# Kernel tuning notes

Measured on AMD Instinct MI355X. Metric: run time of the kernel, lower is better.

Reference implementation:

```python
import jax, jax.numpy as jnp
import numpy as np

VOCAB = 50000
WORD_DIM = 300
ENT_DIM = 128
ATT_DIM = 256
B, QLEN, DLEN = 64, 32, 2048
MUS = np.array([-0.9, -0.7, -0.5, -0.3, -0.1, 0.1, 0.3, 0.5, 0.7, 0.9, 1.0], dtype=np.float32)
SIGMAS = np.array([0.1] * 10 + [0.001], dtype=np.float32)


def setup_inputs() -> dict:
    key = jax.random.key(0)
    ks = jax.random.split(key, 12)
    # tokens in [-1, VOCAB-2]; -1 is padding (embed uses tok+1)
    query_tok = jax.random.randint(ks[0], (B, QLEN), -1, VOCAB - 1)
    doc_tok = jax.random.randint(ks[1], (B, DLEN), -1, VOCAB - 1)
    query_entity = jax.random.normal(ks[2], (B, QLEN, ENT_DIM), dtype=jnp.float32)
    doc_entity = jax.random.normal(ks[3], (B, DLEN, ENT_DIM), dtype=jnp.float32)
    embed_table = jax.random.normal(ks[4], (VOCAB, WORD_DIM), dtype=jnp.float32) * 0.1
    W_t = jax.random.normal(ks[5], (WORD_DIM, ATT_DIM), dtype=jnp.float32) * (1.0 / np.sqrt(WORD_DIM))
    b_t = jax.random.normal(ks[6], (ATT_DIM,), dtype=jnp.float32) * 0.01
    W_e = jax.random.normal(ks[7], (ENT_DIM, ATT_DIM), dtype=jnp.float32) * (1.0 / np.sqrt(ENT_DIM))
    b_e = jax.random.normal(ks[8], (ATT_DIM,), dtype=jnp.float32) * 0.01
    W_c = jax.random.normal(ks[9], (len(MUS), 1), dtype=jnp.float32) * 0.3
    b_c = jax.random.normal(ks[10], (1,), dtype=jnp.float32) * 0.01
    return {
        "query_tok": query_tok, "doc_tok": doc_tok,
        "query_entity": query_entity, "doc_entity": doc_entity,
        "embed_table": embed_table,
        "W_t": W_t, "b_t": b_t, "W_e": W_e, "b_e": b_e,
        "W_c": W_c, "b_c": b_c,
    }


def reference(query_tok, doc_tok, query_entity, doc_entity,
              embed_table, W_t, b_t, W_e, b_e, W_c, b_c):
    mus = jnp.asarray(MUS)
    sigmas = jnp.asarray(SIGMAS)
    # encode: embed(tok + 1)
    q_reps = embed_table[query_tok + 1]            # [B,Q,WORD]
    d_reps = embed_table[doc_tok + 1]              # [B,D,WORD]
    # transform_embed: relu(Linear(word) + Linear(entity))
    q = jax.nn.relu(q_reps @ W_t + b_t + query_entity @ W_e + b_e)  # [B,Q,A]
    d = jax.nn.relu(d_reps @ W_t + b_t + doc_entity @ W_e + b_e)    # [B,D,A]
    # SimmatModule: masked cosine similarity, VIEWS = 1
    qn = jnp.linalg.norm(q, axis=2)[:, :, None] + 1e-9              # [B,Q,1]
    dn = jnp.linalg.norm(d, axis=2)[:, None, :] + 1e-9              # [B,1,D]
    sim = jnp.einsum('bqa,bda->bqd', q, d) / (qn * dn)              # [B,Q,D]
    sim = jnp.where(query_tok[:, :, None] == -1, 0.0, sim)
    sim = jnp.where(doc_tok[:, None, :] == -1, 0.0, sim)
    # RBF kernel bank: exp(-0.5*(sim-mu)^2/sigma^2) -> [B,K,Q,D]
    adj = sim[:, None, :, :] - mus[None, :, None, None]
    kern = jnp.exp(-0.5 * adj * adj / (sigmas * sigmas)[None, :, None, None])
    result = kern.sum(axis=3)                                       # [B,K,Q]
    mask = (sim.sum(axis=2) != 0.0)[:, None, :]                     # [B,1,Q]
    mask = jnp.broadcast_to(mask, result.shape)
    result = jnp.where(mask, jnp.log(result + 1e-6), mask.astype(result.dtype))
    result = result.sum(axis=2)                                     # [B,K]
    scores = result @ W_c + b_c                                     # [B,1]
    return scores
```

## Files before the change

kernel.cpp:

```cpp
#include <hip/hip_runtime.h>
#include <math.h>

#define B_    64
#define QLEN  32
#define DLEN  2048
#define WORD  300
#define ENT   128
#define AD    256
#define NK    11
#define VOCAB 50000

typedef __bf16 bf16x8 __attribute__((ext_vector_type(8)));
typedef __bf16 bf16x4 __attribute__((ext_vector_type(4)));
typedef float  f32x4  __attribute__((ext_vector_type(4)));

__global__ __launch_bounds__(256) void knrm_wpack(
    const float* __restrict__ Wt, const float* __restrict__ We,
    const float* __restrict__ bt, const float* __restrict__ be,
    __bf16* __restrict__ Wtp, __bf16* __restrict__ Wep,
    float* __restrict__ bias)
{
    const int idx = blockIdx.x * 256 + threadIdx.x;
    if (idx < AD) bias[idx] = bt[idx] + be[idx];
    const int tile = idx >> 6, l = idx & 63;
    bf16x8 h;
    if (tile < 160) {
        const int s = tile >> 4, nb = tile & 15;
        const int col = nb * 16 + (l & 15);
        const int k0  = s * 32 + (l >> 4) * 8;
        #pragma unroll
        for (int j = 0; j < 8; ++j) {
            const int k = k0 + j;
            h[j] = (__bf16)((k < WORD) ? Wt[(size_t)k * AD + col] : 0.f);
        }
        *(bf16x8*)((char*)Wtp + (size_t)idx * 16) = h;
    } else {
        const int t2 = tile - 160;
        const int s = t2 >> 4, nb = t2 & 15;
        const int col = nb * 16 + (l & 15);
        const int k0  = s * 32 + (l >> 4) * 8;
        #pragma unroll
        for (int j = 0; j < 8; ++j)
            h[j] = (__bf16)We[(size_t)(k0 + j) * AD + col];
        *(bf16x8*)((char*)Wep + (size_t)(idx - 10240) * 16) = h;
    }
}

__global__ __launch_bounds__(256) void knrm_pgemm(
    const float* __restrict__ emb,
    const __bf16* __restrict__ Wtp,
    char* __restrict__ P)
{
    __shared__ __align__(16) char sm[40960];
    const int tid = threadIdx.x;
    const int v0  = blockIdx.x * 64;

    #pragma unroll
    for (int u = 0; u < 20; ++u) {
        const int idx  = u * 256 + tid;
        const int r    = idx / 80;
        const int slot = idx - r * 80;
        const int k    = slot * 4;
        f32x4 v = (f32x4){0.f, 0.f, 0.f, 0.f};
        if (k < WORD && v0 + r < VOCAB)
            v = *(const f32x4*)(emb + (size_t)(v0 + r) * WORD + k);
        bf16x4 hv;
        #pragma unroll
        for (int c = 0; c < 4; ++c) hv[c] = (__bf16)v[c];
        *(bf16x4*)(sm + ((r * 640 + slot * 8) ^ ((r & 7) << 4))) = hv;
    }
    __syncthreads();

    const int w  = tid >> 6;
    const int l  = tid & 63;
    const int lr = l & 15;
    const int lg = l >> 4;

    f32x4 acc[4][4];
    #pragma unroll
    for (int mf = 0; mf < 4; ++mf)
        #pragma unroll
        for (int nf = 0; nf < 4; ++nf)
            acc[mf][nf] = (f32x4){0.f, 0.f, 0.f, 0.f};

    #pragma unroll
    for (int t = 0; t < 10; ++t) {
        bf16x8 a[4];
        #pragma unroll
        for (int mf = 0; mf < 4; ++mf) {
            const int row = mf * 16 + lr;
            a[mf] = *(const bf16x8*)(sm +
                ((row * 640 + t * 64 + lg * 16) ^ ((row & 7) << 4)));
        }
        bf16x8 wv[4];
        #pragma unroll
        for (int nf = 0; nf < 4; ++nf) {
            const int tile = t * 16 + w * 4 + nf;
            wv[nf] = *(const bf16x8*)((const char*)Wtp + (size_t)tile * 1024 + l * 16);
        }
        #pragma unroll
        for (int mf = 0; mf < 4; ++mf)
            #pragma unroll
            for (int nf = 0; nf < 4; ++nf)
                acc[mf][nf] = __builtin_amdgcn_mfma_f32_16x16x32_bf16(
                    a[mf], wv[nf], acc[mf][nf], 0, 0, 0);
    }

    #pragma unroll
    for (int mf = 0; mf < 4; ++mf)
        #pragma unroll
        for (int reg = 0; reg < 4; ++reg) {
            const int v = v0 + mf * 16 + lg * 4 + reg;
            if (v < VOCAB) {
                bf16x4 h;
                #pragma unroll
                for (int nf = 0; nf < 4; ++nf) h[nf] = (__bf16)acc[mf][nf][reg];
                *(bf16x4*)(P + (size_t)v * 512 + w * 128 + lr * 8) = h;
            }
        }
}

__global__ __launch_bounds__(256) void knrm_qtrans(
    const int* __restrict__ tok,
    const float* __restrict__ ent,
    const char* __restrict__ Pp,
    const __bf16* __restrict__ Wep,
    const float* __restrict__ bias,
    char* __restrict__ qhatF)
{
    __shared__ __align__(16) char sm[16384 + 256];
    float* ssq  = (float*)(sm + 16384);
    int*   toks = (int*)(sm + 16384 + 128);

    const int tid  = threadIdx.x;
    const int row0 = blockIdx.x * 32;
    if (tid < 32) { toks[tid] = tok[row0 + tid] + 1; ssq[tid] = 0.f; }
    __syncthreads();

    const int wN = tid >> 6;
    const int l  = tid & 63;
    const int lr = l & 15;
    const int lg = l >> 4;
    const float* __restrict__ ebase = ent + (size_t)row0 * ENT;

    f32x4 acc[2][4];
    #pragma unroll
    for (int mf = 0; mf < 2; ++mf)
        #pragma unroll
        for (int nf = 0; nf < 4; ++nf)
            acc[mf][nf] = (f32x4){0.f, 0.f, 0.f, 0.f};

    bf16x4 pv[2][4];
    #pragma unroll
    for (int mf = 0; mf < 2; ++mf)
        #pragma unroll
        for (int reg = 0; reg < 4; ++reg) {
            const int r = mf * 16 + lg * 4 + reg;
            pv[mf][reg] = *(const bf16x4*)(Pp +
                (size_t)toks[r] * 512 + wN * 128 + lr * 8);
        }

    #pragma unroll
    for (int t = 0; t < 4; ++t) {
        bf16x8 a[2];
        #pragma unroll
        for (int mf = 0; mf < 2; ++mf) {
            const float* rp = ebase + (size_t)(mf * 16 + lr) * ENT + t * 32 + lg * 8;
            const f32x4 u0 = *(const f32x4*)rp;
            const f32x4 u1 = *(const f32x4*)(rp + 4);
            #pragma unroll
            for (int c = 0; c < 4; ++c) {
                a[mf][c]     = (__bf16)u0[c];
                a[mf][c + 4] = (__bf16)u1[c];
            }
        }
        bf16x8 wv[4];
        #pragma unroll
        for (int nf = 0; nf < 4; ++nf) {
            const int tile = t * 16 + wN * 4 + nf;
            wv[nf] = *(const bf16x8*)((const char*)Wep + (size_t)tile * 1024 + l * 16);
        }
        #pragma unroll
        for (int mf = 0; mf < 2; ++mf)
            #pragma unroll
            for (int nf = 0; nf < 4; ++nf)
                acc[mf][nf] = __builtin_amdgcn_mfma_f32_16x16x32_bf16(
                    a[mf], wv[nf], acc[mf][nf], 0, 0, 0);
    }

    float bv[4];
    #pragma unroll
    for (int nf = 0; nf < 4; ++nf) bv[nf] = bias[wN * 64 + nf * 16 + lr];
    float sq[2][4];
    #pragma unroll
    for (int mf = 0; mf < 2; ++mf)
        #pragma unroll
        for (int reg = 0; reg < 4; ++reg) {
            float s = 0.f;
            #pragma unroll
            for (int nf = 0; nf < 4; ++nf) {
                const float v = fmaxf(acc[mf][nf][reg] + (float)pv[mf][reg][nf]
                                      + bv[nf], 0.f);
                acc[mf][nf][reg] = v;
                s = fmaf(v, v, s);
            }
            sq[mf][reg] = s;
        }
    #pragma unroll
    for (int m = 1; m <= 8; m <<= 1)
        #pragma unroll
        for (int mf = 0; mf < 2; ++mf)
            #pragma unroll
            for (int reg = 0; reg < 4; ++reg)
                sq[mf][reg] += __shfl_xor(sq[mf][reg], m, 64);
    if (lr == 0) {
        #pragma unroll
        for (int mf = 0; mf < 2; ++mf)
            #pragma unroll
            for (int reg = 0; reg < 4; ++reg)
                atomicAdd(&ssq[mf * 16 + lg * 4 + reg], sq[mf][reg]);
    }
    #pragma unroll
    for (int mf = 0; mf < 2; ++mf)
        #pragma unroll
        for (int nf = 0; nf < 4; ++nf)
            #pragma unroll
            for (int reg = 0; reg < 4; ++reg) {
                const int r    = mf * 16 + lg * 4 + reg;
                const int col  = wN * 64 + nf * 16 + lr;
                const int byte = (r * 512 + col * 2) ^ ((r & 7) << 4);
                *(__bf16*)(sm + byte) = (__bf16)acc[mf][nf][reg];
            }
    __syncthreads();

    char* qb = qhatF + (size_t)blockIdx.x * 16384;
    #pragma unroll
    for (int it = 0; it < 4; ++it) {
        const int idx = it * 256 + tid;
        const int tile = idx >> 6, l2 = idx & 63;
        const int s  = tile >> 1, qt = tile & 1;
        const int row = qt * 16 + (l2 & 15);
        const int k0  = s * 32 + (l2 >> 4) * 8;
        const int byte = (row * 512 + k0 * 2) ^ ((row & 7) << 4);
        bf16x8 hv = *(const bf16x8*)(sm + byte);
        const float rn = (toks[row] == 0) ? 0.f
                                          : 1.f / (sqrtf(ssq[row]) + 1e-9f);
        #pragma unroll
        for (int j = 0; j < 8; ++j) hv[j] = (__bf16)((float)hv[j] * rn);
        *(bf16x8*)(qb + tile * 1024 + l2 * 16) = hv;
    }
}

__global__ __launch_bounds__(256) void knrm_fused2(
    const int* __restrict__ dtok,
    const float* __restrict__ dent,
    const char* __restrict__ Pp,
    const __bf16* __restrict__ Wep,
    const float* __restrict__ bias,
    const char* __restrict__ qhatF,
    float* __restrict__ ksum,
    float* __restrict__ simsum)
{
    __shared__ __align__(16) char sm[16384 + 256];
    float* ssq  = (float*)(sm + 16384);
    int*   toks = (int*)(sm + 16384 + 128);

    const int tid = threadIdx.x;
    const int b   = blockIdx.y;
    const int d0  = blockIdx.x * 32;
    const int drow0 = b * DLEN + d0;
    const int w  = tid >> 6;
    const int l  = tid & 63;
    const int lr = l & 15;
    const int lg = l >> 4;

    if (tid < 32) { toks[tid] = dtok[drow0 + tid] + 1; ssq[tid] = 0.f; }

    #pragma unroll
    for (int u = 0; u < 4; ++u) {
        const int slot = u * 256 + tid;
        const int r    = slot >> 5;
        const int c4   = (slot & 31) * 4;
        const f32x4 v = *(const f32x4*)(dent + (size_t)(drow0 + r) * ENT + c4);
        bf16x4 hv;
        #pragma unroll
        for (int c = 0; c < 4; ++c) hv[c] = (__bf16)v[c];
        *(bf16x4*)(sm + ((r * 256 + c4 * 2) ^ ((r & 7) << 4))) = hv;
    }
    __syncthreads();

    bf16x4 pv[2][4];
    #pragma unroll
    for (int mf = 0; mf < 2; ++mf)
        #pragma unroll
        for (int reg = 0; reg < 4; ++reg) {
            const int doc = mf * 16 + lg * 4 + reg;
            pv[mf][reg] = *(const bf16x4*)(Pp +
                (size_t)toks[doc] * 512 + w * 128 + lr * 8);
        }

    f32x4 acc[2][4];
    #pragma unroll
    for (int mf = 0; mf < 2; ++mf)
        #pragma unroll
        for (int nf = 0; nf < 4; ++nf)
            acc[mf][nf] = (f32x4){0.f, 0.f, 0.f, 0.f};

    #pragma unroll
    for (int t = 0; t < 4; ++t) {
        bf16x8 a[2];
        #pragma unroll
        for (int mf = 0; mf < 2; ++mf) {
            const int row = mf * 16 + lr;
            a[mf] = *(const bf16x8*)(sm +
                ((row * 256 + t * 64 + lg * 16) ^ ((row & 7) << 4)));
        }
        bf16x8 wv[4];
        #pragma unroll
        for (int nf = 0; nf < 4; ++nf) {
            const int tile = t * 16 + w * 4 + nf;
            wv[nf] = *(const bf16x8*)((const char*)Wep + (size_t)tile * 1024 + l * 16);
        }
        #pragma unroll
        for (int mf = 0; mf < 2; ++mf)
            #pragma unroll
            for (int nf = 0; nf < 4; ++nf)
                acc[mf][nf] = __builtin_amdgcn_mfma_f32_16x16x32_bf16(
                    a[mf], wv[nf], acc[mf][nf], 0, 0, 0);
    }
    __syncthreads();

    float bv[4];
    #pragma unroll
    for (int nf = 0; nf < 4; ++nf) bv[nf] = bias[w * 64 + nf * 16 + lr];
    float sq[2][4];
    #pragma unroll
    for (int mf = 0; mf < 2; ++mf)
        #pragma unroll
        for (int reg = 0; reg < 4; ++reg) {
            float s = 0.f;
            #pragma unroll
            for (int nf = 0; nf < 4; ++nf) {
                const float v = fmaxf(acc[mf][nf][reg] + (float)pv[mf][reg][nf]
                                      + bv[nf], 0.f);
                acc[mf][nf][reg] = v;
                s = fmaf(v, v, s);
            }
            sq[mf][reg] = s;
        }
    #pragma unroll
    for (int m = 1; m <= 8; m <<= 1)
        #pragma unroll
        for (int mf = 0; mf < 2; ++mf)
            #pragma unroll
            for (int reg = 0; reg < 4; ++reg)
                sq[mf][reg] += __shfl_xor(sq[mf][reg], m, 64);
    if (lr == 0) {
        #pragma unroll
        for (int mf = 0; mf < 2; ++mf)
            #pragma unroll
            for (int reg = 0; reg < 4; ++reg)
                atomicAdd(&ssq[mf * 16 + lg * 4 + reg], sq[mf][reg]);
    }
    #pragma unroll
    for (int mf = 0; mf < 2; ++mf)
        #pragma unroll
        for (int nf = 0; nf < 4; ++nf)
            #pragma unroll
            for (int reg = 0; reg < 4; ++reg) {
                const int doc  = mf * 16 + lg * 4 + reg;
                const int col  = w * 64 + nf * 16 + lr;
                const int byte = doc * 512 + ((col * 2) ^ ((doc & 15) << 4));
                *(__bf16*)(sm + byte) = (__bf16)acc[mf][nf][reg];
            }
    __syncthreads();

    const int dtile = w & 1, qtile = w >> 1;
    const int tdoc  = dtile * 16 + lr;
    const int q     = qtile * 16 + lr;
    const char* __restrict__ qb = qhatF + (size_t)b * 16384;
    f32x4 s0 = (f32x4){0.f, 0.f, 0.f, 0.f};
    #pragma unroll
    for (int s = 0; s < 8; ++s) {
        const bf16x8 ta = *(const bf16x8*)(sm +
            (tdoc * 512 + ((s * 64 + lg * 16) ^ ((tdoc & 15) << 4))));
        const bf16x8 qv = *(const bf16x8*)(qb + (s * 2 + qtile) * 1024 + l * 16);
        s0 = __builtin_amdgcn_mfma_f32_16x16x32_bf16(ta, qv, s0, 0, 0, 0);
    }

    float kq[12];
    #pragma unroll
    for (int k = 0; k < 12; ++k) kq[k] = 0.f;
    #pragma unroll
    for (int reg = 0; reg < 4; ++reg) {
        const int doc = dtile * 16 + lg * 4 + reg;
        const float dnv = (toks[doc] == 0) ? 0.f
                                           : 1.f / (sqrtf(ssq[doc]) + 1e-9f);
        const float sv = s0[reg] * dnv;
        kq[11] += sv;
        const float v5 = __expf(fmaf(10.f, sv, -50.f * sv * sv));
        const float gU = __expf(20.f * sv);
        const float gD = __expf(-20.f * sv);
        float u = v5;
        kq[5] += u * 0.60653066f;
        u *= gD; kq[4] += u * 0.60653066f;
        u *= gD; kq[3] += u * 0.011108997f;
        u *= gD; kq[2] += u * 3.7266532e-06f;
        u *= gD; kq[1] += u * 2.2895532e-11f;
        u *= gD; kq[0] += u * 2.5767571e-18f;
        u = v5;
        u *= gU; kq[6] += u * 0.011108997f;
        u *= gU; kq[7] += u * 3.7266532e-06f;
        u *= gU; kq[8] += u * 2.2895532e-11f;
        u *= gU; kq[9] += u * 2.5767571e-18f;
        const float t10 = sv - 1.0f;
        kq[10] += __expf(-500000.f * t10 * t10);
    }
    #pragma unroll
    for (int m = 16; m <= 32; m <<= 1)
        #pragma unroll
        for (int k = 0; k < 12; ++k)
            kq[k] += __shfl_xor(kq[k], m, 64);
    if (lg == 0) {
        #pragma unroll
        for (int k = 0; k < NK; ++k)
            atomicAdd(&ksum[((size_t)b * NK + k) * QLEN + q], kq[k]);
        atomicAdd(&simsum[b * QLEN + q], kq[11]);
    }
}

__global__ __launch_bounds__(384) void knrm_final(
    const float* __restrict__ ksum,
    const float* __restrict__ simsum,
    const float* __restrict__ Wc, const float* __restrict__ bc,
    float* __restrict__ out)
{
    __shared__ float redq[NK][QLEN];
    __shared__ float res[NK];
    const int b = blockIdx.x;
    const int t = threadIdx.x;
    if (t < NK * QLEN) {
        const int k = t >> 5;
        const int q = t & 31;
        const float ms = simsum[b * QLEN + q];
        redq[k][q] = (ms != 0.0f)
            ? logf(ksum[((size_t)b * NK + k) * QLEN + q] + 1e-6f)
            : 0.0f;
    }
    __syncthreads();
    if (t < NK) {
        float s = 0.f;
        for (int q = 0; q < QLEN; ++q) s += redq[t][q];
        res[t] = s;
    }
    __syncthreads();
    if (t == 0) {
        float s = bc[0];
        for (int k = 0; k < NK; ++k) s += res[k] * Wc[k];
        out[b] = s;
    }
}

extern "C" void kernel_launch(void* const* d_in, const int* in_sizes, int n_in,
                              void* d_out, int out_size, void* d_ws, size_t ws_size,
                              hipStream_t stream)
{
    (void)in_sizes; (void)n_in; (void)out_size; (void)ws_size;
    const int*   qtok = (const int*)d_in[0];
    const int*   dtok = (const int*)d_in[1];
    const float* qent = (const float*)d_in[2];
    const float* dent = (const float*)d_in[3];
    const float* emb  = (const float*)d_in[4];
    const float* Wt   = (const float*)d_in[5];
    const float* bt   = (const float*)d_in[6];
    const float* We   = (const float*)d_in[7];
    const float* be   = (const float*)d_in[8];
    const float* Wc   = (const float*)d_in[9];
    const float* bc   = (const float*)d_in[10];
    float* out = (float*)d_out;

    char* ws = (char*)d_ws;
    const size_t off_qhat = 0;
    const size_t off_Wtp  = off_qhat + 1048576;
    const size_t off_Wep  = off_Wtp  + 163840;
    const size_t off_bias = off_Wep  + 65536;
    const size_t off_ksum = off_bias + 1024;
    const size_t off_sim  = off_ksum + 90112;
    const size_t off_P    = off_sim  + 8192;

    char*   qhatF = ws + off_qhat;
    __bf16* Wtp   = (__bf16*)(ws + off_Wtp);
    __bf16* Wep   = (__bf16*)(ws + off_Wep);
    float*  bias  = (float*)(ws + off_bias);
    float*  ksum  = (float*)(ws + off_ksum);
    float*  simsum= (float*)(ws + off_sim);
    char*   P     = ws + off_P;

    hipMemsetAsync(ksum, 0, (size_t)(90112 + 8192), stream);

    knrm_wpack<<<dim3(56), dim3(256), 0, stream>>>(Wt, We, bt, be, Wtp, Wep, bias);
    knrm_pgemm<<<dim3((VOCAB + 63) / 64), dim3(256), 0, stream>>>(emb, Wtp, P);
    knrm_qtrans<<<dim3(64), dim3(256), 0, stream>>>(
        qtok, qent, P, Wep, bias, qhatF);
    knrm_fused2<<<dim3(DLEN / 32, B_), dim3(256), 0, stream>>>(
        dtok, dent, P, Wep, bias, qhatF, ksum, simsum);
    knrm_final<<<dim3(B_), dim3(384), 0, stream>>>(ksum, simsum, Wc, bc, out);
}
```

Before: 90.52 us.

## Split RBF kernel-bank reduction out of fused doc kernel via bf16 sim buffer

The fused doc kernel now only computes cosine similarities and writes them as bf16 to a workspace buffer. A new kernel reads that buffer, evaluates the RBF kernel bank, reduces through shared memory and then issues far fewer global atomics. The fused kernel also gets a launch-bounds occupancy hint, and the sharp mu=1 kernel is skipped unless sim exceeds 0.98. This trades an extra 8 MB round trip and bf16 rounding of sim values for less register pressure and fewer global atomics.

Result: faster. 84.47 us (median of 2 runs) (-6.7%).

```diff
diff --git a/kernel.cpp b/kernel.cpp
--- a/kernel.cpp
+++ b/kernel.cpp
@@ -251,15 +251,14 @@
     }
 }
 
-__global__ __launch_bounds__(256) void knrm_fused2(
+__global__ __launch_bounds__(256, 4) void knrm_fused5(
     const int* __restrict__ dtok,
     const float* __restrict__ dent,
     const char* __restrict__ Pp,
     const __bf16* __restrict__ Wep,
     const float* __restrict__ bias,
     const char* __restrict__ qhatF,
-    float* __restrict__ ksum,
-    float* __restrict__ simsum)
+    __bf16* __restrict__ simsO)
 {
     __shared__ __align__(16) char sm[16384 + 256];
     float* ssq  = (float*)(sm + 16384);
@@ -377,7 +376,6 @@
 
     const int dtile = w & 1, qtile = w >> 1;
     const int tdoc  = dtile * 16 + lr;
-    const int q     = qtile * 16 + lr;
     const char* __restrict__ qb = qhatF + (size_t)b * 16384;
     f32x4 s0 = (f32x4){0.f, 0.f, 0.f, 0.f};
     #pragma unroll
@@ -388,44 +386,73 @@
         s0 = __builtin_amdgcn_mfma_f32_16x16x32_bf16(ta, qv, s0, 0, 0, 0);
     }
 
-    float kq[12];
-    #pragma unroll
-    for (int k = 0; k < 12; ++k) kq[k] = 0.f;
+    __bf16* so = simsO + ((size_t)b * DLEN + d0) * QLEN;
     #pragma unroll
     for (int reg = 0; reg < 4; ++reg) {
         const int doc = dtile * 16 + lg * 4 + reg;
         const float dnv = (toks[doc] == 0) ? 0.f
                                            : 1.f / (sqrtf(ssq[doc]) + 1e-9f);
-        const float sv = s0[reg] * dnv;
+        so[(size_t)doc * QLEN + qtile * 16 + lr] = (__bf16)(s0[reg] * dnv);
+    }
+}
+
+__global__ __launch_bounds__(256) void knrm_rbf(
+    const __bf16* __restrict__ simsI,
+    float* __restrict__ ksum,
+    float* __restrict__ simsum)
+{
+    __shared__ float red[384];
+    const int tid = threadIdx.x;
+    const int b   = blockIdx.y;
+    const int d0  = blockIdx.x * 128;
+    const int q   = tid & 31;
+    for (int i = tid; i < 384; i += 256) red[i] = 0.f;
+    __syncthreads();
+
+    const __bf16* __restrict__ base = simsI + ((size_t)b * DLEN + d0) * QLEN;
+    float kq[12];
+    #pragma unroll
+    for (int k = 0; k < 12; ++k) kq[k] = 0.f;
+
+    #pragma unroll
+    for (int u = 0; u < 16; ++u) {
+        const float sv = (float)base[u * 256 + tid];
         kq[11] += sv;
         const float v5 = __expf(fmaf(10.f, sv, -50.f * sv * sv));
         const float gU = __expf(20.f * sv);
         const float gD = __expf(-20.f * sv);
-        float u = v5;
-        kq[5] += u * 0.60653066f;
-        u *= gD; kq[4] += u * 0.60653066f;
-        u *= gD; kq[3] += u * 0.011108997f;
-        u *= gD; kq[2] += u * 3.7266532e-06f;
-        u *= gD; kq[1] += u * 2.2895532e-11f;
-        u *= gD; kq[0] += u * 2.5767571e-18f;
-        u = v5;
-        u *= gU; kq[6] += u * 0.011108997f;
-        u *= gU; kq[7] += u * 3.7266532e-06f;
-        u *= gU; kq[8] += u * 2.2895532e-11f;
-        u *= gU; kq[9] += u * 2.5767571e-18f;
-        const float t10 = sv - 1.0f;
-        kq[10] += __expf(-500000.f * t10 * t10);
-    }
-    #pragma unroll
-    for (int m = 16; m <= 32; m <<= 1)
+        float t = v5;
+        kq[5] += t * 0.60653066f;
+        t *= gD; kq[4] += t * 0.60653066f;
+        t *= gD; kq[3] += t * 0.011108997f;
+        t *= gD; kq[2] += t * 3.7266532e-06f;
+        t *= gD; kq[1] += t * 2.2895532e-11f;
+        t *= gD; kq[0] += t * 2.5767571e-18f;
+        t = v5;
+        t *= gU; kq[6] += t * 0.011108997f;
+        t *= gU; kq[7] += t * 3.7266532e-06f;
+        t *= gU; kq[8] += t * 2.2895532e-11f;
+        t *= gU; kq[9] += t * 2.5767571e-18f;
+        if (sv > 0.98f) {
+            const float t10 = sv - 1.0f;
+            kq[10] += __expf(-500000.f * t10 * t10);
+        }
+    }
+
+    #pragma unroll
+    for (int k = 0; k < 12; ++k)
+        kq[k] += __shfl_xor(kq[k], 32, 64);
+    if ((tid & 63) < 32) {
         #pragma unroll
         for (int k = 0; k < 12; ++k)
-            kq[k] += __shfl_xor(kq[k], m, 64);
-    if (lg == 0) {
-        #pragma unroll
-        for (int k = 0; k < NK; ++k)
-            atomicAdd(&ksum[((size_t)b * NK + k) * QLEN + q], kq[k]);
-        atomicAdd(&simsum[b * QLEN + q], kq[11]);
+            atomicAdd(&red[k * 32 + q], kq[k]);
+    }
+    __syncthreads();
+
+    for (int i = tid; i < 384; i += 256) {
+        const int k = i >> 5, qq = i & 31;
+        if (k < NK) atomicAdd(&ksum[((size_t)b * NK + k) * QLEN + qq], red[i]);
+        else        atomicAdd(&simsum[b * QLEN + qq], red[i]);
     }
 }
 
@@ -487,6 +514,7 @@
     const size_t off_ksum = off_bias + 1024;
     const size_t off_sim  = off_ksum + 90112;
     const size_t off_P    = off_sim  + 8192;
+    const size_t off_sims = off_P    + 25600000;
 
     char*   qhatF = ws + off_qhat;
     __bf16* Wtp   = (__bf16*)(ws + off_Wtp);
@@ -495,6 +523,7 @@
     float*  ksum  = (float*)(ws + off_ksum);
     float*  simsum= (float*)(ws + off_sim);
     char*   P     = ws + off_P;
+    __bf16* simsX = (__bf16*)(ws + off_sims);
 
     hipMemsetAsync(ksum, 0, (size_t)(90112 + 8192), stream);
 
@@ -502,7 +531,8 @@
     knrm_pgemm<<<dim3((VOCAB + 63) / 64), dim3(256), 0, stream>>>(emb, Wtp, P);
     knrm_qtrans<<<dim3(64), dim3(256), 0, stream>>>(
         qtok, qent, P, Wep, bias, qhatF);
-    knrm_fused2<<<dim3(DLEN / 32, B_), dim3(256), 0, stream>>>(
-        dtok, dent, P, Wep, bias, qhatF, ksum, simsum);
+    knrm_fused5<<<dim3(DLEN / 32, B_), dim3(256), 0, stream>>>(
+        dtok, dent, P, Wep, bias, qhatF, simsX);
+    knrm_rbf<<<dim3(16, B_), dim3(256), 0, stream>>>(simsX, ksum, simsum);
     knrm_final<<<dim3(B_), dim3(384), 0, stream>>>(ksum, simsum, Wc, bc, out);
 }
```
